# Optimization experiments

Hardware: AMD Instinct MI355X
Metric: run time of the kernel (lower is better)

Reference implementation:

```python
import jax, jax.numpy as jnp
import numpy as np

POS_KL_W = 0.1
NEG_KL_W = 0.02
ORDER_W = 0.5
N_BINS = 1000
SIGMA = 0.1
EPS = 1e-09


def setup_inputs() -> dict:
    key = jax.random.key(0)
    k1, k2, k3 = jax.random.split(key, 3)
    N, D, C = 256, 512, 16
    T_F = jax.random.normal(k1, (N, D), dtype=jnp.float32)
    S_F = jax.random.normal(k2, (N, D), dtype=jnp.float32)
    labels = jax.random.uniform(k3, (N, C), dtype=jnp.float32)  # argmax -> class ids
    return {"T_F": T_F, "S_F": S_F, "labels": labels}


def _histograms_and_means(x, pos_labels, neg_labels, t):
    # x: [N, D]; L2-normalize rows (eps matches F.normalize default 1e-12)
    norm = jnp.maximum(jnp.linalg.norm(x, axis=-1, keepdims=True), 1e-12)
    xn = x / norm
    cos = xn @ xn.T                      # [N, N]
    dists = cos.reshape(-1)              # [N*N]
    # Gaussian soft-binning: [N*N, N_BINS] (the big memory-bound intermediate)
    delta = jnp.exp(-0.5 * ((dists[:, None] - t[None, :]) / SIGMA) ** 2)
    neg_w = neg_labels.reshape(-1)
    pos_w = pos_labels.reshape(-1)
    neg_p = (neg_w @ delta) / jnp.sum(neg_w)   # [N_BINS]
    pos_p = (pos_w @ delta) / jnp.sum(pos_w)   # [N_BINS]
    E_pos = jnp.sum(cos * pos_labels, axis=-1) / jnp.sum(pos_labels, axis=-1)  # [N]
    E_neg = jnp.sum(cos * neg_labels, axis=-1) / jnp.sum(neg_labels, axis=-1)  # [N]
    return neg_p, pos_p, E_neg, E_pos


def _kl(anchor, dist):
    # torch F.kl_div(log(dist+eps), anchor+eps, reduction='batchmean'); batch dim is 1
    a = anchor + EPS
    d = dist + EPS
    return jnp.sum(a * (jnp.log(a) - jnp.log(d)))


def reference(T_F, S_F, labels):
    N = T_F.shape[0]
    t = jnp.arange(-1.0, 1.0, 2.0 / N_BINS, dtype=jnp.float32)  # [1000] bin centers
    lab = jnp.argmax(labels, axis=-1)                            # [N]
    grid = (lab[None, :] == lab[:, None]).astype(jnp.float32)    # [N, N]
    neg_labels = 1.0 - grid
    pos_labels = grid * (1.0 - jnp.eye(N, dtype=jnp.float32))

    neg_t, pos_t, E_neg_t, E_pos_t = _histograms_and_means(T_F, pos_labels, neg_labels, t)
    neg_s, pos_s, E_neg_s, E_pos_s = _histograms_and_means(S_F, pos_labels, neg_labels, t)

    pos_kl = POS_KL_W * _kl(pos_t, pos_s)
    neg_kl = NEG_KL_W * _kl(neg_t, neg_s)
    o1 = jnp.mean(jnp.abs(E_pos_t - E_pos_s))
    o2 = jnp.mean(jnp.abs(E_neg_t - E_neg_s))
    o3 = jnp.mean(E_pos_s - E_neg_s)
    order_loss = ORDER_W * (o1 + o2 + o3)
    return pos_kl + neg_kl + order_loss
```

## Files before the change

kernel.cpp:

```cpp
#include <hip/hip_runtime.h>
#include <hip/hip_bf16.h>
#include <math.h>

#define N 256
#define D 512
#define C 16
#define NBINS 1000
#define MCELL 1000
#define MSTRIDE 1024
#define EPSF 1e-9f
#define KEXP2 -72.134752f
#define NCB 32

__device__ inline float waveReduceSum(float v) {
#pragma unroll
    for (int off = 32; off > 0; off >>= 1) v += __shfl_down(v, off, 64);
    return v;
}
__device__ inline double waveReduceSumD(double v) {
#pragma unroll
    for (int off = 32; off > 0; off >>= 1) v += __shfl_down(v, off, 64);
    return v;
}

__global__ void k_norm(const float* __restrict__ T, const float* __restrict__ S,
                       const float* __restrict__ labels,
                       float* __restrict__ xn, float* __restrict__ xnT,
                       int* __restrict__ lab, float* __restrict__ mg) {
    int i = blockIdx.x;
    int mat = blockIdx.y;
    int tid = threadIdx.x;
    if (mat == 1 && i < 12) {
        ((float4*)(mg + i * 1024))[tid] = make_float4(0.f, 0.f, 0.f, 0.f);
    }
    const float* in = mat ? S : T;
    if (mat == 0 && tid == 0) {
        float best = labels[i * C];
        int bi = 0;
#pragma unroll
        for (int c = 1; c < C; ++c) {
            float v = labels[i * C + c];
            if (v > best) { best = v; bi = c; }
        }
        lab[i] = bi;
    }
    float v0 = in[i * D + tid];
    float v1 = in[i * D + 256 + tid];
    float ss = v0 * v0 + v1 * v1;
    ss = waveReduceSum(ss);
    __shared__ float lds[4];
    __shared__ float inv_s;
    int wid = tid >> 6, lane = tid & 63;
    if (lane == 0) lds[wid] = ss;
    __syncthreads();
    if (tid == 0) {
        float tot = lds[0] + lds[1] + lds[2] + lds[3];
        inv_s = 1.0f / fmaxf(sqrtf(tot), 1e-12f);
    }
    __syncthreads();
    float inv = inv_s;
    float* xnm = xn + mat * (N * D);
    float* xnTm = xnT + mat * (N * D);
    float a = v0 * inv, b = v1 * inv;
    xnm[i * D + tid] = a;
    xnm[i * D + 256 + tid] = b;
    xnTm[tid * N + i] = a;
    xnTm[(tid + 256) * N + i] = b;
}

__global__ void __launch_bounds__(256) k_cos(
        const float* __restrict__ xn, const float* __restrict__ xnT,
        const int* __restrict__ lab, float* __restrict__ mg,
        float* __restrict__ Earr, float* __restrict__ cpos) {
    int mat = blockIdx.y;
    int i0 = blockIdx.x * 4;
    int j = threadIdx.x;
    const float* xnm = xn + mat * (N * D);
    const float* xc = xnT + mat * (N * D);
    __shared__ float rows[D][4];
    __shared__ float mom[6 * 1024];
    for (int i = j; i < 6 * 1024; i += 256) mom[i] = 0.f;
#pragma unroll
    for (int r = 0; r < 4; ++r) {
        rows[j][r] = xnm[(i0 + r) * D + j];
        rows[j + 256][r] = xnm[(i0 + r) * D + 256 + j];
    }
    int labj = lab[j];
    int li0 = lab[i0], li1 = lab[i0 + 1], li2 = lab[i0 + 2], li3 = lab[i0 + 3];
    __syncthreads();

    float a0 = 0.f, a1 = 0.f, a2 = 0.f, a3 = 0.f;
#pragma unroll 8
    for (int k = 0; k < D; ++k) {
        float xb = xc[k * N + j];
        float4 rr = *(const float4*)&rows[k][0];
        a0 = fmaf(rr.x, xb, a0);
        a1 = fmaf(rr.y, xb, a1);
        a2 = fmaf(rr.z, xb, a2);
        a3 = fmaf(rr.w, xb, a3);
    }
    float av[4] = {a0, a1, a2, a3};
    int liv[4] = {li0, li1, li2, li3};
    float wp[4], vA[4];
#pragma unroll
    for (int r = 0; r < 4; ++r) {
        bool diag = (j == i0 + r);
        wp[r] = (labj == liv[r] && !diag) ? 1.f : 0.f;
        vA[r] = diag ? 0.f : av[r];
        if (!diag) {
            float d = av[r];
            int jc = (int)floorf((d + 1.f) * 500.f);
            jc = max(0, min(jc, MCELL - 1));
            float del = d - (-1.f + ((float)jc + 0.5f) * 0.002f);
            float dd = del * del;
            atomicAdd(&mom[jc], 1.f);
            atomicAdd(&mom[MSTRIDE + jc], del);
            atomicAdd(&mom[2 * MSTRIDE + jc], dd);
            if (wp[r] > 0.f) {
                atomicAdd(&mom[3 * MSTRIDE + jc], 1.f);
                atomicAdd(&mom[4 * MSTRIDE + jc], del);
                atomicAdd(&mom[5 * MSTRIDE + jc], dd);
            }
        }
    }

    float r0 = waveReduceSum(vA[0]);
    float r1 = waveReduceSum(av[0] * wp[0]);
    float r2 = waveReduceSum(wp[0]);
    float r3 = waveReduceSum(vA[1]);
    float r4 = waveReduceSum(av[1] * wp[1]);
    float r5 = waveReduceSum(wp[1]);
    float r6 = waveReduceSum(vA[2]);
    float r7 = waveReduceSum(av[2] * wp[2]);
    float r8 = waveReduceSum(wp[2]);
    float r9 = waveReduceSum(vA[3]);
    float r10 = waveReduceSum(av[3] * wp[3]);
    float r11 = waveReduceSum(wp[3]);
    __shared__ float red[4][12];
    int wid = j >> 6, lane = j & 63;
    if (lane == 0) {
        red[wid][0] = r0;  red[wid][1] = r1;  red[wid][2] = r2;
        red[wid][3] = r3;  red[wid][4] = r4;  red[wid][5] = r5;
        red[wid][6] = r6;  red[wid][7] = r7;  red[wid][8] = r8;
        red[wid][9] = r9;  red[wid][10] = r10; red[wid][11] = r11;
    }
    __syncthreads();

    for (int i = j; i < 6 * 1024; i += 256) {
        float v = mom[i];
        if (v != 0.f) atomicAdd(&mg[mat * 6144 + i], v);
    }
    if (j < 4) {
        float sA = 0, sP = 0, cP = 0;
        for (int w = 0; w < 4; ++w) {
            sA += red[w][j * 3 + 0];
            sP += red[w][j * 3 + 1];
            cP += red[w][j * 3 + 2];
        }
        int row = i0 + j;
        Earr[(mat * 2 + 0) * N + row] = sP / cP;
        Earr[(mat * 2 + 1) * N + row] = (sA - sP) / (255.f - cP);
        if (mat == 0) cpos[row] = cP;
    }
}

__global__ void __launch_bounds__(1024) k_conv(const float* __restrict__ mg,
                                               float* __restrict__ hpp,
                                               float* __restrict__ hss) {
    int mat = blockIdx.y, b = blockIdx.x;
    int tid = threadIdx.x;
    int c0 = b * 32;
    __shared__ float sm[6][32];
    if (tid < 192) {
        int m = tid >> 5, c = tid & 31;
        sm[m][c] = mg[mat * 6144 + m * MSTRIDE + c0 + c];
    }
    __syncthreads();
    float tb = -1.f + 0.002f * (float)tid;
    float pa = 0.f, sa = 0.f;
#pragma unroll 4
    for (int cc = 0; cc < 32; ++cc) {
        float m0 = sm[0][cc];
        if (m0 == 0.f) continue;
        float cj = -1.f + ((float)(c0 + cc) + 0.5f) * 0.002f;
        float q = cj - tb;
        float q2 = q * q;
        if (q2 < 0.5f) {
            float E = __builtin_amdgcn_exp2f(KEXP2 * q2);
            float u = 100.f * q;
            float w2 = fmaf(0.5f * u, u, -50.f);
            sa = fmaf(E, fmaf(w2, sm[2][cc], fmaf(-u, sm[1][cc], m0)), sa);
            pa = fmaf(E, fmaf(w2, sm[5][cc], fmaf(-u, sm[4][cc], sm[3][cc])), pa);
        }
    }
    if (tid < NBINS) {
        hpp[(mat * NCB + b) * NBINS + tid] = pa;
        hss[(mat * NCB + b) * NBINS + tid] = sa;
    }
}

__global__ void __launch_bounds__(1024) k_final(const float* __restrict__ hpp,
                                                const float* __restrict__ hss,
                                                const float* __restrict__ Earr,
                                                const float* __restrict__ cpos,
                                                float* __restrict__ out) {
    int tid = threadIdx.x;
    int wid = tid >> 6, lane = tid & 63;
    __shared__ float cred[16];
    __shared__ float pcnt_s;
    float cv = (tid < N) ? cpos[tid] : 0.f;
    cv = waveReduceSum(cv);
    if (lane == 0) cred[wid] = cv;
    __syncthreads();
    if (tid == 0) {
        float t = 0;
        for (int w = 0; w < 16; ++w) t += cred[w];
        pcnt_s = t;
    }
    __syncthreads();
    float pcnt = pcnt_s;
    float ncnt = 65280.f - pcnt;

    double poskl = 0, negkl = 0, o1 = 0, o2 = 0, o3 = 0;
    if (tid < NBINS) {
        float hpT = 0, hsT = 0, hpS = 0, hsS = 0;
#pragma unroll 8
        for (int b = 0; b < NCB; ++b) {
            hpT += hpp[(0 * NCB + b) * NBINS + tid];
            hsT += hss[(0 * NCB + b) * NBINS + tid];
            hpS += hpp[(1 * NCB + b) * NBINS + tid];
            hsS += hss[(1 * NCB + b) * NBINS + tid];
        }
        float pt = hpT / pcnt;
        float nt = (hsT - hpT) / ncnt;
        float ps = hpS / pcnt;
        float ns = (hsS - hpS) / ncnt;
        poskl = (double)((pt + EPSF) * (__logf(pt + EPSF) - __logf(ps + EPSF)));
        negkl = (double)((nt + EPSF) * (__logf(nt + EPSF) - __logf(ns + EPSF)));
    }
    if (tid < N) {
        float ept = Earr[0 * N + tid];
        float ent = Earr[1 * N + tid];
        float eps_ = Earr[2 * N + tid];
        float ens = Earr[3 * N + tid];
        o1 = fabs((double)ept - (double)eps_);
        o2 = fabs((double)ent - (double)ens);
        o3 = (double)eps_ - (double)ens;
    }
    poskl = waveReduceSumD(poskl);
    negkl = waveReduceSumD(negkl);
    o1 = waveReduceSumD(o1);
    o2 = waveReduceSumD(o2);
    o3 = waveReduceSumD(o3);
    __shared__ double lds[16][5];
    if (lane == 0) {
        lds[wid][0] = poskl; lds[wid][1] = negkl;
        lds[wid][2] = o1; lds[wid][3] = o2; lds[wid][4] = o3;
    }
    __syncthreads();
    if (tid == 0) {
        double a = 0, b = 0, c = 0, d = 0, e = 0;
        for (int w = 0; w < 16; ++w) {
            a += lds[w][0]; b += lds[w][1]; c += lds[w][2]; d += lds[w][3]; e += lds[w][4];
        }
        double loss = 0.1 * a + 0.02 * b + 0.5 * ((c + d + e) / (double)N);
        out[0] = (float)loss;
    }
}

extern "C" void kernel_launch(void* const* d_in, const int* in_sizes, int n_in,
                              void* d_out, int out_size, void* d_ws, size_t ws_size,
                              hipStream_t stream) {
    const float* T = (const float*)d_in[0];
    const float* S = (const float*)d_in[1];
    const float* labels = (const float*)d_in[2];
    float* out = (float*)d_out;

    float* ws = (float*)d_ws;
    float* xn = ws;
    float* xnT = xn + 2 * N * D;
    float* mg = xnT + 2 * N * D;
    float* hpp = mg + 2 * 6 * MSTRIDE;
    float* hss = hpp + 2 * NCB * NBINS;
    float* Earr = hss + 2 * NCB * NBINS;
    float* cpos = Earr + 4 * N;
    int* lab = (int*)(cpos + N);

    k_norm<<<dim3(N, 2), 256, 0, stream>>>(T, S, labels, xn, xnT, lab, mg);
    k_cos<<<dim3(N / 4, 2), 256, 0, stream>>>(xn, xnT, lab, mg, Earr, cpos);
    k_conv<<<dim3(NCB, 2), 1024, 0, stream>>>(mg, hpp, hss);
    k_final<<<1, 1024, 0, stream>>>(hpp, hss, Earr, cpos, out);
}
```

Baseline: 53.65 us.

## Fuse all stages into one cooperative kernel with grid syncs

Replaces the four launches (normalize, cosine/moment binning, Gaussian convolution, final reduction) with a single cooperative kernel of 128 blocks separated by grid.sync. Normalization is folded into the dot product by scaling raw dots with per-row inverse norms, so the normalized and transposed copies are no longer written. Global moment atomics are replaced by per-block partial buffers that a second phase reduces deterministically, and the convolution is split across 16 lanes per bin with shuffle reductions. This removes launch overhead and intermediate traffic, but adds grid-wide barrier costs, redundant label argmax in every block, and uncoalesced row-strided float4 loads of X in the dot product.

```diff
diff --git a/kernel.cpp b/kernel.cpp
--- a/kernel.cpp
+++ b/kernel.cpp
@@ -1,16 +1,18 @@
 #include <hip/hip_runtime.h>
-#include <hip/hip_bf16.h>
+#include <hip/hip_cooperative_groups.h>
 #include <math.h>
+
+namespace cg = cooperative_groups;
 
 #define N 256
 #define D 512
 #define C 16
 #define NBINS 1000
 #define MCELL 1000
-#define MSTRIDE 1024
 #define EPSF 1e-9f
 #define KEXP2 -72.134752f
-#define NCB 32
+#define NBLK 128
+#define NTHR 256
 
 __device__ inline float waveReduceSum(float v) {
 #pragma unroll
@@ -23,89 +25,87 @@
     return v;
 }
 
-__global__ void k_norm(const float* __restrict__ T, const float* __restrict__ S,
-                       const float* __restrict__ labels,
-                       float* __restrict__ xn, float* __restrict__ xnT,
-                       int* __restrict__ lab, float* __restrict__ mg) {
-    int i = blockIdx.x;
-    int mat = blockIdx.y;
-    int tid = threadIdx.x;
-    if (mat == 1 && i < 12) {
-        ((float4*)(mg + i * 1024))[tid] = make_float4(0.f, 0.f, 0.f, 0.f);
-    }
-    const float* in = mat ? S : T;
-    if (mat == 0 && tid == 0) {
-        float best = labels[i * C];
+__global__ void __launch_bounds__(NTHR) k_mega(
+        const float* __restrict__ T, const float* __restrict__ S,
+        const float* __restrict__ labels,
+        float* __restrict__ mgp, float* __restrict__ mg,
+        float* __restrict__ hp, float* __restrict__ hs,
+        float* __restrict__ Earr, float* __restrict__ cpos,
+        float* __restrict__ out) {
+    cg::grid_group grid = cg::this_grid();
+    int b = blockIdx.x;
+    int mat = b >> 6;
+    int i0 = (b & 63) << 2;
+    int j = threadIdx.x;
+    int wid = j >> 6, lane = j & 63;
+
+    __shared__ float sm[12288];
+    __shared__ float invs[256];
+    __shared__ int labs[256];
+    __shared__ float red[4][12];
+    __shared__ double dred[4][5];
+
+    const float* X = mat ? S : T;
+
+    {
+        float best = labels[j * C];
         int bi = 0;
 #pragma unroll
         for (int c = 1; c < C; ++c) {
-            float v = labels[i * C + c];
+            float v = labels[j * C + c];
             if (v > best) { best = v; bi = c; }
         }
-        lab[i] = bi;
-    }
-    float v0 = in[i * D + tid];
-    float v1 = in[i * D + 256 + tid];
-    float ss = v0 * v0 + v1 * v1;
-    ss = waveReduceSum(ss);
-    __shared__ float lds[4];
-    __shared__ float inv_s;
-    int wid = tid >> 6, lane = tid & 63;
-    if (lane == 0) lds[wid] = ss;
-    __syncthreads();
-    if (tid == 0) {
-        float tot = lds[0] + lds[1] + lds[2] + lds[3];
-        inv_s = 1.0f / fmaxf(sqrtf(tot), 1e-12f);
-    }
-    __syncthreads();
-    float inv = inv_s;
-    float* xnm = xn + mat * (N * D);
-    float* xnTm = xnT + mat * (N * D);
-    float a = v0 * inv, b = v1 * inv;
-    xnm[i * D + tid] = a;
-    xnm[i * D + 256 + tid] = b;
-    xnTm[tid * N + i] = a;
-    xnTm[(tid + 256) * N + i] = b;
-}
-
-__global__ void __launch_bounds__(256) k_cos(
-        const float* __restrict__ xn, const float* __restrict__ xnT,
-        const int* __restrict__ lab, float* __restrict__ mg,
-        float* __restrict__ Earr, float* __restrict__ cpos) {
-    int mat = blockIdx.y;
-    int i0 = blockIdx.x * 4;
-    int j = threadIdx.x;
-    const float* xnm = xn + mat * (N * D);
-    const float* xc = xnT + mat * (N * D);
-    __shared__ float rows[D][4];
-    __shared__ float mom[6 * 1024];
-    for (int i = j; i < 6 * 1024; i += 256) mom[i] = 0.f;
-#pragma unroll
-    for (int r = 0; r < 4; ++r) {
-        rows[j][r] = xnm[(i0 + r) * D + j];
-        rows[j + 256][r] = xnm[(i0 + r) * D + 256 + j];
-    }
-    int labj = lab[j];
-    int li0 = lab[i0], li1 = lab[i0 + 1], li2 = lab[i0 + 2], li3 = lab[i0 + 3];
-    __syncthreads();
-
-    float a0 = 0.f, a1 = 0.f, a2 = 0.f, a3 = 0.f;
+        labs[j] = bi;
+    }
+    {
+        float4 lo, hi;
+        lo.x = X[(i0 + 0) * D + j];
+        lo.y = X[(i0 + 1) * D + j];
+        lo.z = X[(i0 + 2) * D + j];
+        lo.w = X[(i0 + 3) * D + j];
+        hi.x = X[(i0 + 0) * D + 256 + j];
+        hi.y = X[(i0 + 1) * D + 256 + j];
+        hi.z = X[(i0 + 2) * D + 256 + j];
+        hi.w = X[(i0 + 3) * D + 256 + j];
+        ((float4*)sm)[j] = lo;
+        ((float4*)sm)[j + 256] = hi;
+    }
+    for (int i = j; i < 6144; i += NTHR) sm[2048 + i] = 0.f;
+    __syncthreads();
+
+    float d0 = 0.f, d1 = 0.f, d2 = 0.f, d3 = 0.f, ssq = 0.f;
+    {
+        const float4* xrow = (const float4*)(X + j * D);
+        const float4* rws = (const float4*)sm;
 #pragma unroll 8
-    for (int k = 0; k < D; ++k) {
-        float xb = xc[k * N + j];
-        float4 rr = *(const float4*)&rows[k][0];
-        a0 = fmaf(rr.x, xb, a0);
-        a1 = fmaf(rr.y, xb, a1);
-        a2 = fmaf(rr.z, xb, a2);
-        a3 = fmaf(rr.w, xb, a3);
-    }
-    float av[4] = {a0, a1, a2, a3};
-    int liv[4] = {li0, li1, li2, li3};
+        for (int k4 = 0; k4 < 128; ++k4) {
+            float4 xj = xrow[k4];
+            float4 q0 = rws[4 * k4 + 0];
+            float4 q1 = rws[4 * k4 + 1];
+            float4 q2 = rws[4 * k4 + 2];
+            float4 q3 = rws[4 * k4 + 3];
+            d0 = fmaf(q0.x, xj.x, fmaf(q1.x, xj.y, fmaf(q2.x, xj.z, fmaf(q3.x, xj.w, d0))));
+            d1 = fmaf(q0.y, xj.x, fmaf(q1.y, xj.y, fmaf(q2.y, xj.z, fmaf(q3.y, xj.w, d1))));
+            d2 = fmaf(q0.z, xj.x, fmaf(q1.z, xj.y, fmaf(q2.z, xj.z, fmaf(q3.z, xj.w, d2))));
+            d3 = fmaf(q0.w, xj.x, fmaf(q1.w, xj.y, fmaf(q2.w, xj.z, fmaf(q3.w, xj.w, d3))));
+            ssq = fmaf(xj.x, xj.x, fmaf(xj.y, xj.y, fmaf(xj.z, xj.z, fmaf(xj.w, xj.w, ssq))));
+        }
+    }
+    invs[j] = 1.0f / fmaxf(sqrtf(ssq), 1e-12f);
+    __syncthreads();
+    float invj = invs[j];
+    float av[4];
+    av[0] = d0 * invs[i0 + 0] * invj;
+    av[1] = d1 * invs[i0 + 1] * invj;
+    av[2] = d2 * invs[i0 + 2] * invj;
+    av[3] = d3 * invs[i0 + 3] * invj;
+
+    int labj = labs[j];
     float wp[4], vA[4];
 #pragma unroll
     for (int r = 0; r < 4; ++r) {
         bool diag = (j == i0 + r);
-        wp[r] = (labj == liv[r] && !diag) ? 1.f : 0.f;
+        wp[r] = (labj == labs[i0 + r] && !diag) ? 1.f : 0.f;
         vA[r] = diag ? 0.f : av[r];
         if (!diag) {
             float d = av[r];
@@ -113,43 +113,38 @@
             jc = max(0, min(jc, MCELL - 1));
             float del = d - (-1.f + ((float)jc + 0.5f) * 0.002f);
             float dd = del * del;
-            atomicAdd(&mom[jc], 1.f);
-            atomicAdd(&mom[MSTRIDE + jc], del);
-            atomicAdd(&mom[2 * MSTRIDE + jc], dd);
+            atomicAdd(&sm[2048 + jc], 1.f);
+            atomicAdd(&sm[2048 + 1024 + jc], del);
+            atomicAdd(&sm[2048 + 2048 + jc], dd);
             if (wp[r] > 0.f) {
-                atomicAdd(&mom[3 * MSTRIDE + jc], 1.f);
-                atomicAdd(&mom[4 * MSTRIDE + jc], del);
-                atomicAdd(&mom[5 * MSTRIDE + jc], dd);
+                atomicAdd(&sm[2048 + 3072 + jc], 1.f);
+                atomicAdd(&sm[2048 + 4096 + jc], del);
+                atomicAdd(&sm[2048 + 5120 + jc], dd);
             }
         }
     }
 
-    float r0 = waveReduceSum(vA[0]);
-    float r1 = waveReduceSum(av[0] * wp[0]);
-    float r2 = waveReduceSum(wp[0]);
-    float r3 = waveReduceSum(vA[1]);
-    float r4 = waveReduceSum(av[1] * wp[1]);
-    float r5 = waveReduceSum(wp[1]);
-    float r6 = waveReduceSum(vA[2]);
-    float r7 = waveReduceSum(av[2] * wp[2]);
-    float r8 = waveReduceSum(wp[2]);
-    float r9 = waveReduceSum(vA[3]);
-    float r10 = waveReduceSum(av[3] * wp[3]);
-    float r11 = waveReduceSum(wp[3]);
-    __shared__ float red[4][12];
-    int wid = j >> 6, lane = j & 63;
-    if (lane == 0) {
-        red[wid][0] = r0;  red[wid][1] = r1;  red[wid][2] = r2;
-        red[wid][3] = r3;  red[wid][4] = r4;  red[wid][5] = r5;
-        red[wid][6] = r6;  red[wid][7] = r7;  red[wid][8] = r8;
-        red[wid][9] = r9;  red[wid][10] = r10; red[wid][11] = r11;
-    }
-    __syncthreads();
-
-    for (int i = j; i < 6 * 1024; i += 256) {
-        float v = mom[i];
-        if (v != 0.f) atomicAdd(&mg[mat * 6144 + i], v);
-    }
+    {
+        float r0 = waveReduceSum(vA[0]);
+        float r1 = waveReduceSum(av[0] * wp[0]);
+        float r2 = waveReduceSum(wp[0]);
+        float r3 = waveReduceSum(vA[1]);
+        float r4 = waveReduceSum(av[1] * wp[1]);
+        float r5 = waveReduceSum(wp[1]);
+        float r6 = waveReduceSum(vA[2]);
+        float r7 = waveReduceSum(av[2] * wp[2]);
+        float r8 = waveReduceSum(wp[2]);
+        float r9 = waveReduceSum(vA[3]);
+        float r10 = waveReduceSum(av[3] * wp[3]);
+        float r11 = waveReduceSum(wp[3]);
+        if (lane == 0) {
+            red[wid][0] = r0;  red[wid][1] = r1;  red[wid][2] = r2;
+            red[wid][3] = r3;  red[wid][4] = r4;  red[wid][5] = r5;
+            red[wid][6] = r6;  red[wid][7] = r7;  red[wid][8] = r8;
+            red[wid][9] = r9;  red[wid][10] = r10; red[wid][11] = r11;
+        }
+    }
+    __syncthreads();
     if (j < 4) {
         float sA = 0, sP = 0, cP = 0;
         for (int w = 0; w < 4; ++w) {
@@ -162,87 +157,102 @@
         Earr[(mat * 2 + 1) * N + row] = (sA - sP) / (255.f - cP);
         if (mat == 0) cpos[row] = cP;
     }
-}
-
-__global__ void __launch_bounds__(1024) k_conv(const float* __restrict__ mg,
-                                               float* __restrict__ hpp,
-                                               float* __restrict__ hss) {
-    int mat = blockIdx.y, b = blockIdx.x;
-    int tid = threadIdx.x;
-    int c0 = b * 32;
-    __shared__ float sm[6][32];
-    if (tid < 192) {
-        int m = tid >> 5, c = tid & 31;
-        sm[m][c] = mg[mat * 6144 + m * MSTRIDE + c0 + c];
-    }
-    __syncthreads();
-    float tb = -1.f + 0.002f * (float)tid;
-    float pa = 0.f, sa = 0.f;
-#pragma unroll 4
-    for (int cc = 0; cc < 32; ++cc) {
-        float m0 = sm[0][cc];
-        if (m0 == 0.f) continue;
-        float cj = -1.f + ((float)(c0 + cc) + 0.5f) * 0.002f;
-        float q = cj - tb;
-        float q2 = q * q;
-        if (q2 < 0.5f) {
-            float E = __builtin_amdgcn_exp2f(KEXP2 * q2);
-            float u = 100.f * q;
-            float w2 = fmaf(0.5f * u, u, -50.f);
-            sa = fmaf(E, fmaf(w2, sm[2][cc], fmaf(-u, sm[1][cc], m0)), sa);
-            pa = fmaf(E, fmaf(w2, sm[5][cc], fmaf(-u, sm[4][cc], sm[3][cc])), pa);
-        }
-    }
-    if (tid < NBINS) {
-        hpp[(mat * NCB + b) * NBINS + tid] = pa;
-        hss[(mat * NCB + b) * NBINS + tid] = sa;
-    }
-}
-
-__global__ void __launch_bounds__(1024) k_final(const float* __restrict__ hpp,
-                                                const float* __restrict__ hss,
-                                                const float* __restrict__ Earr,
-                                                const float* __restrict__ cpos,
-                                                float* __restrict__ out) {
-    int tid = threadIdx.x;
-    int wid = tid >> 6, lane = tid & 63;
-    __shared__ float cred[16];
-    __shared__ float pcnt_s;
-    float cv = (tid < N) ? cpos[tid] : 0.f;
+    {
+        float4* dst4 = (float4*)(mgp + (size_t)b * 6144);
+        const float4* src4 = (const float4*)(sm + 2048);
+        for (int i = j; i < 1536; i += NTHR) dst4[i] = src4[i];
+    }
+
+    grid.sync();
+
+    {
+        int g = b * NTHR + j;
+        if (g < 2 * 6144) {
+            int m2 = g >> 13 >= 1 ? 1 : (g >= 6144 ? 1 : 0);
+            m2 = g >= 6144 ? 1 : 0;
+            int idx = g - m2 * 6144;
+            float acc = 0.f;
+            const float* src = mgp + (size_t)m2 * 64 * 6144 + idx;
+#pragma unroll 8
+            for (int s = 0; s < 64; ++s) acc += src[(size_t)s * 6144];
+            mg[g] = acc;
+        }
+    }
+
+    grid.sync();
+
+    for (int i = j; i < 12288; i += NTHR) sm[i] = mg[i];
+    __syncthreads();
+    {
+        int g = b * NTHR + j;
+        int tb = g >> 4;
+        int sub = g & 15;
+        if (tb < 2000) {
+            int m3 = tb >= 1000 ? 1 : 0;
+            int bin = tb - m3 * 1000;
+            float t = -1.f + 0.002f * (float)bin;
+            int base = m3 * 6144;
+            float pa = 0.f, sa = 0.f;
+            for (int c = sub; c < MCELL; c += 16) {
+                float m0 = sm[base + c];
+                if (m0 == 0.f) continue;
+                float cj = -1.f + ((float)c + 0.5f) * 0.002f;
+                float q = cj - t;
+                float q2 = q * q;
+                if (q2 < 0.5f) {
+                    float E = __builtin_amdgcn_exp2f(KEXP2 * q2);
+                    float u = 100.f * q;
+                    float w2 = fmaf(0.5f * u, u, -50.f);
+                    sa = fmaf(E, fmaf(w2, sm[base + 2048 + c],
+                                      fmaf(-u, sm[base + 1024 + c], m0)), sa);
+                    pa = fmaf(E, fmaf(w2, sm[base + 5120 + c],
+                                      fmaf(-u, sm[base + 4096 + c],
+                                           sm[base + 3072 + c])), pa);
+                }
+            }
+#pragma unroll
+            for (int off = 1; off < 16; off <<= 1) {
+                pa += __shfl_xor(pa, off, 16);
+                sa += __shfl_xor(sa, off, 16);
+            }
+            if (sub == 0) {
+                hp[tb] = pa;
+                hs[tb] = sa;
+            }
+        }
+    }
+
+    grid.sync();
+
+    if (b != 0) return;
+
+    float cv = cpos[j];
     cv = waveReduceSum(cv);
-    if (lane == 0) cred[wid] = cv;
-    __syncthreads();
-    if (tid == 0) {
-        float t = 0;
-        for (int w = 0; w < 16; ++w) t += cred[w];
-        pcnt_s = t;
-    }
-    __syncthreads();
-    float pcnt = pcnt_s;
+    if (lane == 0) red[wid][0] = cv;
+    __syncthreads();
+    float pcnt = red[0][0] + red[1][0] + red[2][0] + red[3][0];
     float ncnt = 65280.f - pcnt;
 
-    double poskl = 0, negkl = 0, o1 = 0, o2 = 0, o3 = 0;
-    if (tid < NBINS) {
-        float hpT = 0, hsT = 0, hpS = 0, hsS = 0;
-#pragma unroll 8
-        for (int b = 0; b < NCB; ++b) {
-            hpT += hpp[(0 * NCB + b) * NBINS + tid];
-            hsT += hss[(0 * NCB + b) * NBINS + tid];
-            hpS += hpp[(1 * NCB + b) * NBINS + tid];
-            hsS += hss[(1 * NCB + b) * NBINS + tid];
-        }
-        float pt = hpT / pcnt;
-        float nt = (hsT - hpT) / ncnt;
-        float ps = hpS / pcnt;
-        float ns = (hsS - hpS) / ncnt;
-        poskl = (double)((pt + EPSF) * (__logf(pt + EPSF) - __logf(ps + EPSF)));
-        negkl = (double)((nt + EPSF) * (__logf(nt + EPSF) - __logf(ns + EPSF)));
-    }
-    if (tid < N) {
-        float ept = Earr[0 * N + tid];
-        float ent = Earr[1 * N + tid];
-        float eps_ = Earr[2 * N + tid];
-        float ens = Earr[3 * N + tid];
+    double poskl = 0, negkl = 0, o1, o2, o3;
+#pragma unroll
+    for (int u = 0; u < 4; ++u) {
+        int bin = j + u * 256;
+        if (bin < NBINS) {
+            float hpT = hp[bin], hsT = hs[bin];
+            float hpS = hp[1000 + bin], hsS = hs[1000 + bin];
+            float pt = hpT / pcnt;
+            float nt = (hsT - hpT) / ncnt;
+            float ps = hpS / pcnt;
+            float ns = (hsS - hpS) / ncnt;
+            poskl += (double)((pt + EPSF) * (__logf(pt + EPSF) - __logf(ps + EPSF)));
+            negkl += (double)((nt + EPSF) * (__logf(nt + EPSF) - __logf(ns + EPSF)));
+        }
+    }
+    {
+        float ept = Earr[0 * N + j];
+        float ent = Earr[1 * N + j];
+        float eps_ = Earr[2 * N + j];
+        float ens = Earr[3 * N + j];
         o1 = fabs((double)ept - (double)eps_);
         o2 = fabs((double)ent - (double)ens);
         o3 = (double)eps_ - (double)ens;
@@ -252,18 +262,18 @@
     o1 = waveReduceSumD(o1);
     o2 = waveReduceSumD(o2);
     o3 = waveReduceSumD(o3);
-    __shared__ double lds[16][5];
     if (lane == 0) {
-        lds[wid][0] = poskl; lds[wid][1] = negkl;
-        lds[wid][2] = o1; lds[wid][3] = o2; lds[wid][4] = o3;
-    }
-    __syncthreads();
-    if (tid == 0) {
-        double a = 0, b = 0, c = 0, d = 0, e = 0;
-        for (int w = 0; w < 16; ++w) {
-            a += lds[w][0]; b += lds[w][1]; c += lds[w][2]; d += lds[w][3]; e += lds[w][4];
-        }
-        double loss = 0.1 * a + 0.02 * b + 0.5 * ((c + d + e) / (double)N);
+        dred[wid][0] = poskl; dred[wid][1] = negkl;
+        dred[wid][2] = o1; dred[wid][3] = o2; dred[wid][4] = o3;
+    }
+    __syncthreads();
+    if (j == 0) {
+        double a = 0, bb = 0, c = 0, d = 0, e = 0;
+        for (int w = 0; w < 4; ++w) {
+            a += dred[w][0]; bb += dred[w][1];
+            c += dred[w][2]; d += dred[w][3]; e += dred[w][4];
+        }
+        double loss = 0.1 * a + 0.02 * bb + 0.5 * ((c + d + e) / (double)N);
         out[0] = (float)loss;
     }
 }
@@ -277,17 +287,15 @@
     float* out = (float*)d_out;
 
     float* ws = (float*)d_ws;
-    float* xn = ws;
-    float* xnT = xn + 2 * N * D;
-    float* mg = xnT + 2 * N * D;
-    float* hpp = mg + 2 * 6 * MSTRIDE;
-    float* hss = hpp + 2 * NCB * NBINS;
-    float* Earr = hss + 2 * NCB * NBINS;
-    float* cpos = Earr + 4 * N;
-    int* lab = (int*)(cpos + N);
-
-    k_norm<<<dim3(N, 2), 256, 0, stream>>>(T, S, labels, xn, xnT, lab, mg);
-    k_cos<<<dim3(N / 4, 2), 256, 0, stream>>>(xn, xnT, lab, mg, Earr, cpos);
-    k_conv<<<dim3(NCB, 2), 1024, 0, stream>>>(mg, hpp, hss);
-    k_final<<<1, 1024, 0, stream>>>(hpp, hss, Earr, cpos, out);
+    float* mgp = ws;
+    float* mg = mgp + (size_t)NBLK * 6144;
+    float* hp = mg + 12288;
+    float* hs = hp + 2000;
+    float* Earr = hs + 2000;
+    float* cpos = Earr + 1024;
+
+    void* args[] = {(void*)&T, (void*)&S, (void*)&labels, (void*)&mgp, (void*)&mg,
+                    (void*)&hp, (void*)&hs, (void*)&Earr, (void*)&cpos, (void*)&out};
+    hipLaunchCooperativeKernel((const void*)k_mega, dim3(NBLK), dim3(NTHR),
+                               args, 0, stream);
 }
```

Result: slower. 101.7 us (+89.6%).

## Fuse histogram convolution and final KL reduction into one tail kernel

Applied to the files above, without the earlier changes.

Merges the per-chunk moment-to-bin convolution and the final KL/order-loss reduction into a single 64-block kernel. Each block computes 16 bins directly over all moment cells for both matrices and folds in the KL terms. The last block, found through an atomic counter, does the final reduction. This removes one kernel launch and the partial histogram round trip through global memory. In exchange each block does a longer serial loop over 1000 cells and copies 48KB of moments into LDS.

```diff
diff --git a/kernel.cpp b/kernel.cpp
--- a/kernel.cpp
+++ b/kernel.cpp
@@ -1,5 +1,4 @@
 #include <hip/hip_runtime.h>
-#include <hip/hip_bf16.h>
 #include <math.h>
 
 #define N 256
@@ -10,7 +9,7 @@
 #define MSTRIDE 1024
 #define EPSF 1e-9f
 #define KEXP2 -72.134752f
-#define NCB 32
+#define TAILB 64
 
 __device__ inline float waveReduceSum(float v) {
 #pragma unroll
@@ -23,16 +22,17 @@
     return v;
 }
 
-__global__ void k_norm(const float* __restrict__ T, const float* __restrict__ S,
+__global__ void k_prep(const float* __restrict__ T, const float* __restrict__ S,
                        const float* __restrict__ labels,
                        float* __restrict__ xn, float* __restrict__ xnT,
-                       int* __restrict__ lab, float* __restrict__ mg) {
+                       int* __restrict__ lab, float* __restrict__ mg,
+                       unsigned int* __restrict__ cnt) {
     int i = blockIdx.x;
     int mat = blockIdx.y;
     int tid = threadIdx.x;
-    if (mat == 1 && i < 12) {
-        ((float4*)(mg + i * 1024))[tid] = make_float4(0.f, 0.f, 0.f, 0.f);
-    }
+    int bid = mat * 256 + i;
+    if (bid < 48) mg[bid * 256 + tid] = 0.f;
+    if (bid == 48 && tid == 0) cnt[0] = 0u;
     const float* in = mat ? S : T;
     if (mat == 0 && tid == 0) {
         float best = labels[i * C];
@@ -68,7 +68,7 @@
     xnTm[(tid + 256) * N + i] = b;
 }
 
-__global__ void __launch_bounds__(256) k_cos(
+__global__ void __launch_bounds__(256) k_main(
         const float* __restrict__ xn, const float* __restrict__ xnT,
         const int* __restrict__ lab, float* __restrict__ mg,
         float* __restrict__ Earr, float* __restrict__ cpos) {
@@ -164,81 +164,104 @@
     }
 }
 
-__global__ void __launch_bounds__(1024) k_conv(const float* __restrict__ mg,
-                                               float* __restrict__ hpp,
-                                               float* __restrict__ hss) {
-    int mat = blockIdx.y, b = blockIdx.x;
+__global__ void __launch_bounds__(256) k_tail(const float* __restrict__ mg,
+                                              const float* __restrict__ Earr,
+                                              const float* __restrict__ cpos,
+                                              float* __restrict__ pkl,
+                                              unsigned int* __restrict__ cnt,
+                                              float* __restrict__ out) {
+    int b = blockIdx.x;
     int tid = threadIdx.x;
-    int c0 = b * 32;
-    __shared__ float sm[6][32];
-    if (tid < 192) {
-        int m = tid >> 5, c = tid & 31;
-        sm[m][c] = mg[mat * 6144 + m * MSTRIDE + c0 + c];
-    }
-    __syncthreads();
-    float tb = -1.f + 0.002f * (float)tid;
-    float pa = 0.f, sa = 0.f;
-#pragma unroll 4
-    for (int cc = 0; cc < 32; ++cc) {
-        float m0 = sm[0][cc];
-        if (m0 == 0.f) continue;
-        float cj = -1.f + ((float)(c0 + cc) + 0.5f) * 0.002f;
-        float q = cj - tb;
+    int wid = tid >> 6, lane = tid & 63;
+    __shared__ float sm[12288];
+    __shared__ float binres[16][4];
+    __shared__ float kterm[16][2];
+    __shared__ float credL[4];
+    __shared__ unsigned int old_s;
+    __shared__ double dred[4][5];
+
+    for (int i = tid; i < 3072; i += 256)
+        ((float4*)sm)[i] = ((const float4*)mg)[i];
+
+    float cv = cpos[tid];
+    cv = waveReduceSum(cv);
+    if (lane == 0) credL[wid] = cv;
+    __syncthreads();
+    float pcnt = credL[0] + credL[1] + credL[2] + credL[3];
+    float ncnt = 65280.f - pcnt;
+
+    int u = tid >> 4, sub = tid & 15;
+    int bin = b * 16 + u;
+    float t = -1.f + 0.002f * (float)bin;
+    float paT = 0.f, saT = 0.f, paS = 0.f, saS = 0.f;
+    for (int c = sub; c < MCELL; c += 16) {
+        float m0T = sm[c], m0S = sm[6144 + c];
+        if (m0T == 0.f && m0S == 0.f) continue;
+        float cj = -1.f + ((float)c + 0.5f) * 0.002f;
+        float q = cj - t;
         float q2 = q * q;
         if (q2 < 0.5f) {
             float E = __builtin_amdgcn_exp2f(KEXP2 * q2);
-            float u = 100.f * q;
-            float w2 = fmaf(0.5f * u, u, -50.f);
-            sa = fmaf(E, fmaf(w2, sm[2][cc], fmaf(-u, sm[1][cc], m0)), sa);
-            pa = fmaf(E, fmaf(w2, sm[5][cc], fmaf(-u, sm[4][cc], sm[3][cc])), pa);
-        }
-    }
-    if (tid < NBINS) {
-        hpp[(mat * NCB + b) * NBINS + tid] = pa;
-        hss[(mat * NCB + b) * NBINS + tid] = sa;
-    }
-}
-
-__global__ void __launch_bounds__(1024) k_final(const float* __restrict__ hpp,
-                                                const float* __restrict__ hss,
-                                                const float* __restrict__ Earr,
-                                                const float* __restrict__ cpos,
-                                                float* __restrict__ out) {
-    int tid = threadIdx.x;
-    int wid = tid >> 6, lane = tid & 63;
-    __shared__ float cred[16];
-    __shared__ float pcnt_s;
-    float cv = (tid < N) ? cpos[tid] : 0.f;
-    cv = waveReduceSum(cv);
-    if (lane == 0) cred[wid] = cv;
+            float u1 = 100.f * q;
+            float w2 = fmaf(0.5f * u1, u1, -50.f);
+            saT = fmaf(E, fmaf(w2, sm[2048 + c], fmaf(-u1, sm[1024 + c], m0T)), saT);
+            paT = fmaf(E, fmaf(w2, sm[5120 + c], fmaf(-u1, sm[4096 + c], sm[3072 + c])), paT);
+            saS = fmaf(E, fmaf(w2, sm[6144 + 2048 + c], fmaf(-u1, sm[6144 + 1024 + c], m0S)), saS);
+            paS = fmaf(E, fmaf(w2, sm[6144 + 5120 + c], fmaf(-u1, sm[6144 + 4096 + c], sm[6144 + 3072 + c])), paS);
+        }
+    }
+#pragma unroll
+    for (int off = 1; off < 16; off <<= 1) {
+        paT += __shfl_xor(paT, off, 16);
+        saT += __shfl_xor(saT, off, 16);
+        paS += __shfl_xor(paS, off, 16);
+        saS += __shfl_xor(saS, off, 16);
+    }
+    if (sub == 0) {
+        binres[u][0] = paT; binres[u][1] = saT;
+        binres[u][2] = paS; binres[u][3] = saS;
+    }
+    __syncthreads();
+
+    if (tid < 16) {
+        int bn = b * 16 + tid;
+        float pk = 0.f, nk = 0.f;
+        if (bn < NBINS) {
+            float hpT = binres[tid][0], hsT = binres[tid][1];
+            float hpS = binres[tid][2], hsS = binres[tid][3];
+            float pt = hpT / pcnt;
+            float nt = (hsT - hpT) / ncnt;
+            float ps = hpS / pcnt;
+            float ns = (hsS - hpS) / ncnt;
+            pk = (pt + EPSF) * (__logf(pt + EPSF) - __logf(ps + EPSF));
+            nk = (nt + EPSF) * (__logf(nt + EPSF) - __logf(ns + EPSF));
+        }
+        kterm[tid][0] = pk;
+        kterm[tid][1] = nk;
+    }
     __syncthreads();
     if (tid == 0) {
-        float t = 0;
-        for (int w = 0; w < 16; ++w) t += cred[w];
-        pcnt_s = t;
-    }
-    __syncthreads();
-    float pcnt = pcnt_s;
-    float ncnt = 65280.f - pcnt;
-
-    double poskl = 0, negkl = 0, o1 = 0, o2 = 0, o3 = 0;
-    if (tid < NBINS) {
-        float hpT = 0, hsT = 0, hpS = 0, hsS = 0;
-#pragma unroll 8
-        for (int b = 0; b < NCB; ++b) {
-            hpT += hpp[(0 * NCB + b) * NBINS + tid];
-            hsT += hss[(0 * NCB + b) * NBINS + tid];
-            hpS += hpp[(1 * NCB + b) * NBINS + tid];
-            hsS += hss[(1 * NCB + b) * NBINS + tid];
-        }
-        float pt = hpT / pcnt;
-        float nt = (hsT - hpT) / ncnt;
-        float ps = hpS / pcnt;
-        float ns = (hsS - hpS) / ncnt;
-        poskl = (double)((pt + EPSF) * (__logf(pt + EPSF) - __logf(ps + EPSF)));
-        negkl = (double)((nt + EPSF) * (__logf(nt + EPSF) - __logf(ns + EPSF)));
-    }
-    if (tid < N) {
+        float a = 0.f, bb = 0.f;
+        for (int q = 0; q < 16; ++q) { a += kterm[q][0]; bb += kterm[q][1]; }
+        pkl[b * 2] = a;
+        pkl[b * 2 + 1] = bb;
+        __threadfence();
+        old_s = atomicAdd(cnt, 1u);
+    }
+    __syncthreads();
+    if (old_s != TAILB - 1) return;
+
+    __threadfence();
+    double a = 0.0, bb = 0.0;
+    if (tid < TAILB) {
+        volatile const float* vp = pkl;
+        a = (double)vp[2 * tid];
+        bb = (double)vp[2 * tid + 1];
+    }
+    a = waveReduceSumD(a);
+    bb = waveReduceSumD(bb);
+    double o1, o2, o3;
+    {
         float ept = Earr[0 * N + tid];
         float ent = Earr[1 * N + tid];
         float eps_ = Earr[2 * N + tid];
@@ -247,23 +270,21 @@
         o2 = fabs((double)ent - (double)ens);
         o3 = (double)eps_ - (double)ens;
     }
-    poskl = waveReduceSumD(poskl);
-    negkl = waveReduceSumD(negkl);
     o1 = waveReduceSumD(o1);
     o2 = waveReduceSumD(o2);
     o3 = waveReduceSumD(o3);
-    __shared__ double lds[16][5];
     if (lane == 0) {
-        lds[wid][0] = poskl; lds[wid][1] = negkl;
-        lds[wid][2] = o1; lds[wid][3] = o2; lds[wid][4] = o3;
+        dred[wid][0] = a;  dred[wid][1] = bb;
+        dred[wid][2] = o1; dred[wid][3] = o2; dred[wid][4] = o3;
     }
     __syncthreads();
     if (tid == 0) {
-        double a = 0, b = 0, c = 0, d = 0, e = 0;
-        for (int w = 0; w < 16; ++w) {
-            a += lds[w][0]; b += lds[w][1]; c += lds[w][2]; d += lds[w][3]; e += lds[w][4];
-        }
-        double loss = 0.1 * a + 0.02 * b + 0.5 * ((c + d + e) / (double)N);
+        double A = dred[0][0], B = dred[0][1];
+        double Co = 0, Do = 0, Eo = 0;
+        for (int w = 0; w < 4; ++w) {
+            Co += dred[w][2]; Do += dred[w][3]; Eo += dred[w][4];
+        }
+        double loss = 0.1 * A + 0.02 * B + 0.5 * ((Co + Do + Eo) / (double)N);
         out[0] = (float)loss;
     }
 }
@@ -280,14 +301,13 @@
     float* xn = ws;
     float* xnT = xn + 2 * N * D;
     float* mg = xnT + 2 * N * D;
-    float* hpp = mg + 2 * 6 * MSTRIDE;
-    float* hss = hpp + 2 * NCB * NBINS;
-    float* Earr = hss + 2 * NCB * NBINS;
-    float* cpos = Earr + 4 * N;
-    int* lab = (int*)(cpos + N);
-
-    k_norm<<<dim3(N, 2), 256, 0, stream>>>(T, S, labels, xn, xnT, lab, mg);
-    k_cos<<<dim3(N / 4, 2), 256, 0, stream>>>(xn, xnT, lab, mg, Earr, cpos);
-    k_conv<<<dim3(NCB, 2), 1024, 0, stream>>>(mg, hpp, hss);
-    k_final<<<1, 1024, 0, stream>>>(hpp, hss, Earr, cpos, out);
-}
+    float* Earr = mg + 12288;
+    float* cpos = Earr + 1024;
+    float* pkl = cpos + 256;
+    unsigned int* cnt = (unsigned int*)(pkl + 128);
+    int* lab = (int*)(cnt + 1);
+
+    k_prep<<<dim3(N, 2), 256, 0, stream>>>(T, S, labels, xn, xnT, lab, mg, cnt);
+    k_main<<<dim3(N / 4, 2), 256, 0, stream>>>(xn, xnT, lab, mg, Earr, cpos);
+    k_tail<<<TAILB, 256, 0, stream>>>(mg, Earr, cpos, pkl, cnt, out);
+}
```

Result: faster. 52.56 us (-2.0%).
